# Optimization experiments

Hardware: AMD Instinct MI355X
Metric: run time of the kernel (lower is better)

Reference implementation:

```python
import jax, jax.numpy as jnp
import numpy as np

N = 50000
E = 1600000
IN_C = 256
HID = 32
HEADS = 4
NUM_CLASSES = 16
NEG_SLOPE = 0.2  # PyG GATConv default leaky_relu slope


def setup_inputs() -> dict:
    key = jax.random.key(0)
    ks = jax.random.split(key, 12)
    glorot = lambda k, shape: jax.random.normal(k, shape, jnp.float32) * jnp.sqrt(2.0 / (shape[0] + shape[-1]))
    x = jax.random.normal(ks[0], (N, IN_C), jnp.float32)
    edge_index = jax.random.randint(ks[1], (2, E), 0, N, jnp.int64)
    # layer 1: in -> hidden x heads, concat
    W1 = glorot(ks[2], (IN_C, HEADS * HID))
    att_src1 = glorot(ks[3], (HEADS, HID))
    att_dst1 = glorot(ks[4], (HEADS, HID))
    b1 = jnp.zeros((HEADS * HID,), jnp.float32)
    # layer 2: hidden*heads -> num_classes, 1 head, no concat
    W2 = glorot(ks[5], (HEADS * HID, NUM_CLASSES))
    att_src2 = glorot(ks[6], (1, NUM_CLASSES))
    att_dst2 = glorot(ks[7], (1, NUM_CLASSES))
    b2 = jnp.zeros((NUM_CLASSES,), jnp.float32)
    return {"x": x, "edge_index": edge_index, "W1": W1, "att_src1": att_src1,
            "att_dst1": att_dst1, "b1": b1, "W2": W2, "att_src2": att_src2,
            "att_dst2": att_dst2, "b2": b2}


def gat_conv(x, src, dst, W, a_src, a_dst, b, concat):
    # x: [N, F_in]; src/dst: [E'] (self-loops included); a_src/a_dst: [H, C]
    H, C = a_src.shape
    h = (x @ W).reshape(-1, H, C)                       # [N, H, C]
    alpha_s = jnp.sum(h * a_src[None], axis=-1)          # [N, H]
    alpha_d = jnp.sum(h * a_dst[None], axis=-1)          # [N, H]
    e = jax.nn.leaky_relu(alpha_s[src] + alpha_d[dst], NEG_SLOPE)  # [E', H]
    # segment softmax over edges grouped by destination node
    m = jax.ops.segment_max(e, dst, num_segments=N)      # [N, H]
    m = jnp.where(jnp.isfinite(m), m, 0.0)
    p = jnp.exp(e - m[dst])
    denom = jax.ops.segment_sum(p, dst, num_segments=N)  # [N, H]
    coef = p / (denom[dst] + 1e-16)                      # [E', H]
    msg = h[src] * coef[:, :, None]                      # [E', H, C]
    out = jax.ops.segment_sum(msg, dst, num_segments=N)  # [N, H, C]
    out = out.reshape(N, H * C) if concat else out.mean(axis=1)
    return out + b


def reference(x, edge_index, W1, att_src1, att_dst1, b1, W2, att_src2, att_dst2, b2):
    # PyG GATConv adds self-loops by default
    loops = jnp.arange(N, dtype=edge_index.dtype)
    src = jnp.concatenate([edge_index[0], loops])
    dst = jnp.concatenate([edge_index[1], loops])
    h = gat_conv(x, src, dst, W1, att_src1, att_dst1, b1, concat=True)
    h = jax.nn.elu(h)
    # dropout is identity in eval mode
    out = gat_conv(h, src, dst, W2, att_src2, att_dst2, b2, concat=False)
    return jax.nn.log_softmax(out, axis=1)
```

## Files before the change

### kernel.cpp

```cpp
#include <hip/hip_runtime.h>
#include <math.h>

#define INC   256
#define HIDALL 128
#define HEADS 4
#define HID   32
#define NCLS  16
#define NEG   0.2f
#define BSH   9
#define MAXBUCK 128
#define BCAP  24576

typedef __attribute__((ext_vector_type(8))) short short8_t;
typedef __attribute__((ext_vector_type(4))) float f32x4_t;

__device__ __forceinline__ float lrelu(float v) { return fmaxf(v, NEG * v); }

__device__ __forceinline__ float bflo(unsigned int v) { return __uint_as_float(v << 16); }
__device__ __forceinline__ float bfhi(unsigned int v) { return __uint_as_float(v & 0xFFFF0000u); }
__device__ __forceinline__ float bfhix(unsigned int v) { return __uint_as_float(v); }
__device__ __forceinline__ unsigned int f2bf(float f) {
  unsigned int v = __float_as_uint(f);
  return (v + 0x7FFFu + ((v >> 16) & 1u)) >> 16;
}
__device__ __forceinline__ unsigned int pack2(float a, float b) {
  return f2bf(a) | (f2bf(b) << 16);
}

__global__ void wt_k(const float* __restrict__ W, unsigned short* __restrict__ wtb) {
  int i = blockIdx.x * 256 + threadIdx.x;
  int k = i >> 7, c = i & 127;
  wtb[(((k >> 5) * 4 + ((k >> 3) & 3)) * 128 + c) * 8 + (k & 7)] =
      (unsigned short)f2bf(W[i]);
}

#define GM 64
__global__ __launch_bounds__(256) void gemm1_k(const float* __restrict__ x,
                                               const unsigned short* __restrict__ wtb,
                                               const float* __restrict__ asrc,
                                               const float* __restrict__ adst,
                                               unsigned short* __restrict__ h1,
                                               float* __restrict__ as1,
                                               float* __restrict__ ad1, int Nrows) {
  __shared__ unsigned short xs2[4][GM][8];
  __shared__ unsigned short wsm2[4][128][8];
  __shared__ unsigned short hs[GM][128];
  __shared__ float attL[2 * HIDALL];
  int t = threadIdx.x;
  int m0 = blockIdx.x * GM;
  int w = t >> 6, lane = t & 63;
  if (t < HIDALL) attL[t] = asrc[t];
  else attL[t] = adst[t - HIDALL];

  f32x4_t acc[8];
#pragma unroll
  for (int ct = 0; ct < 8; ++ct) acc[ct] = (f32x4_t){0.f, 0.f, 0.f, 0.f};

  int rowA = w * 16 + (lane & 15);
  int kg = lane >> 4;
  int cl = lane & 15;

  for (int ks = 0; ks < 8; ++ks) {
    int kc = ks * 32;
#pragma unroll
    for (int jj = 0; jj < 2; ++jj) {
      int u = t + jj * 256;
      int row = u >> 3, c4i = u & 7;
      int gr = m0 + row;
      float4 v = (gr < Nrows) ? *(const float4*)&x[(size_t)gr * INC + kc + c4i * 4]
                              : make_float4(0.f, 0.f, 0.f, 0.f);
      uint2 p;
      p.x = pack2(v.x, v.y);
      p.y = pack2(v.z, v.w);
      *(uint2*)&xs2[c4i >> 1][row][(c4i & 1) * 4] = p;
    }
    const unsigned short* wt = wtb + ks * 4096;
#pragma unroll
    for (int jj = 0; jj < 2; ++jj) {
      int u = t + jj * 256;
      *(uint4*)&((unsigned short*)wsm2)[u * 8] = *(const uint4*)&wt[u * 8];
    }
    __syncthreads();
    short8_t a = *(const short8_t*)&xs2[kg][rowA][0];
#pragma unroll
    for (int ct = 0; ct < 8; ++ct) {
      short8_t b = *(const short8_t*)&wsm2[kg][ct * 16 + cl][0];
      acc[ct] = __builtin_amdgcn_mfma_f32_16x16x32_bf16(a, b, acc[ct], 0, 0, 0);
    }
    __syncthreads();
  }
#pragma unroll
  for (int ct = 0; ct < 8; ++ct)
#pragma unroll
    for (int r = 0; r < 4; ++r)
      hs[w * 16 + (lane >> 4) * 4 + r][ct * 16 + cl] = (unsigned short)f2bf(acc[ct][r]);
  __syncthreads();
#pragma unroll
  for (int jj = 0; jj < 4; ++jj) {
    int u = t + jj * 256;
    int row = u >> 4, seg = u & 15;
    int gr = m0 + row;
    if (gr < Nrows)
      *(uint4*)&h1[(size_t)gr * HIDALL + seg * 8] = *(const uint4*)&hs[row][seg * 8];
  }
  {
    int row = t >> 2, h = t & 3;
    int gr = m0 + row;
    if (gr < Nrows) {
      float s = 0.f, dd = 0.f;
#pragma unroll
      for (int qq = 0; qq < 4; ++qq) {
        uint4 qv = *(const uint4*)&hs[row][h * 32 + qq * 8];
        int ab = h * 32 + qq * 8;
        s = fmaf(bflo(qv.x), attL[ab + 0], s);
        dd = fmaf(bflo(qv.x), attL[HIDALL + ab + 0], dd);
        s = fmaf(bfhi(qv.x), attL[ab + 1], s);
        dd = fmaf(bfhi(qv.x), attL[HIDALL + ab + 1], dd);
        s = fmaf(bflo(qv.y), attL[ab + 2], s);
        dd = fmaf(bflo(qv.y), attL[HIDALL + ab + 2], dd);
        s = fmaf(bfhi(qv.y), attL[ab + 3], s);
        dd = fmaf(bfhi(qv.y), attL[HIDALL + ab + 3], dd);
        s = fmaf(bflo(qv.z), attL[ab + 4], s);
        dd = fmaf(bflo(qv.z), attL[HIDALL + ab + 4], dd);
        s = fmaf(bfhi(qv.z), attL[ab + 5], s);
        dd = fmaf(bfhi(qv.z), attL[HIDALL + ab + 5], dd);
        s = fmaf(bflo(qv.w), attL[ab + 6], s);
        dd = fmaf(bflo(qv.w), attL[HIDALL + ab + 6], dd);
        s = fmaf(bfhi(qv.w), attL[ab + 7], s);
        dd = fmaf(bfhi(qv.w), attL[HIDALL + ab + 7], dd);
      }
      as1[(size_t)gr * 4 + h] = s;
      ad1[(size_t)gr * 4 + h] = dd;
    }
  }
}

#define S1_CH 8
__global__ __launch_bounds__(256) void stage1_k(const int* __restrict__ ei, int E,
                                                int* __restrict__ cursor,
                                                unsigned int* __restrict__ staging) {
  __shared__ int bh[MAXBUCK];
  __shared__ int bb[MAXBUCK];
  int t = threadIdx.x;
  if (t < MAXBUCK) bh[t] = 0;
  __syncthreads();
  int base = blockIdx.x * (256 * S1_CH);
  int s[S1_CH], d[S1_CH], r[S1_CH];
#pragma unroll
  for (int j = 0; j < S1_CH; ++j) {
    int e = base + t + j * 256;
    if (e < E) {
      s[j] = ei[e];
      d[j] = ei[(size_t)E + e];
      r[j] = atomicAdd(&bh[d[j] >> BSH], 1);
    } else {
      d[j] = -1;
    }
  }
  __syncthreads();
  if (t < MAXBUCK && bh[t]) bb[t] = atomicAdd(&cursor[t], bh[t]);
  __syncthreads();
#pragma unroll
  for (int j = 0; j < S1_CH; ++j) {
    if (d[j] >= 0) {
      int b = d[j] >> BSH;
      staging[(size_t)b * BCAP + bb[b] + r[j]] = ((unsigned)d[j] << 16) | (unsigned)s[j];
    }
  }
}

__global__ __launch_bounds__(MAXBUCK) void bscan_k(const int* __restrict__ cursor,
                                                   int* __restrict__ bucketOff) {
  __shared__ int v[MAXBUCK];
  int t = threadIdx.x;
  v[t] = cursor[t];
  __syncthreads();
  for (int off = 1; off < MAXBUCK; off <<= 1) {
    int x = (t >= off) ? v[t - off] : 0;
    __syncthreads();
    v[t] += x;
    __syncthreads();
  }
  bucketOff[t] = t ? v[t - 1] : 0;
  if (t == MAXBUCK - 1) bucketOff[MAXBUCK] = v[t];
}

__global__ __launch_bounds__(1024) void stage2_k(const unsigned int* __restrict__ staging,
                                                 const int* __restrict__ bucketOff,
                                                 int* __restrict__ rowptr,
                                                 int* __restrict__ esrc, int n, int lastb) {
  __shared__ int cnt[1 << BSH];
  __shared__ int cur[1 << BSH];
  int b = blockIdx.x, nb0 = b << BSH, t = threadIdx.x;
  if (t < (1 << BSH)) cnt[t] = 0;
  __syncthreads();
  int gbeg = bucketOff[b];
  int fill = bucketOff[b + 1] - gbeg;
  const unsigned int* st = staging + (size_t)b * BCAP;
  for (int i = t; i < fill; i += 1024)
    atomicAdd(&cnt[(st[i] >> 16) - nb0], 1);
  __syncthreads();
  for (int o = 1; o < (1 << BSH); o <<= 1) {
    int v = 0;
    if (t < (1 << BSH) && t >= o) v = cnt[t - o];
    __syncthreads();
    if (t < (1 << BSH)) cnt[t] += v;
    __syncthreads();
  }
  if (t < (1 << BSH)) {
    int excl = t ? cnt[t - 1] : 0;
    int node = nb0 + t;
    if (node < n) rowptr[node] = gbeg + excl;
    cur[t] = gbeg + excl;
  }
  if (b == lastb && t == 0) rowptr[n] = bucketOff[b + 1];
  __syncthreads();
  for (int i = t; i < fill; i += 1024) {
    unsigned v = st[i];
    int pos = atomicAdd(&cur[(v >> 16) - nb0], 1);
    esrc[pos] = (int)(v & 0xFFFFu);
  }
}

#define A1FMA(w_, u_)                                                      \
  a[0] = fmaf(w_, bflo(u_.x), a[0]); a[1] = fmaf(w_, bfhix(u_.x), a[1]);   \
  a[2] = fmaf(w_, bflo(u_.y), a[2]); a[3] = fmaf(w_, bfhix(u_.y), a[3]);   \
  a[4] = fmaf(w_, bflo(u_.z), a[4]); a[5] = fmaf(w_, bfhix(u_.z), a[5]);   \
  a[6] = fmaf(w_, bflo(u_.w), a[6]); a[7] = fmaf(w_, bfhix(u_.w), a[7]);

__global__ __launch_bounds__(256) void agg1_k(const int* __restrict__ rowptr,
                                              const int* __restrict__ esrc,
                                              const unsigned short* __restrict__ h1,
                                              const float* __restrict__ as1,
                                              const float* __restrict__ ad1,
                                              const float* __restrict__ b1,
                                              unsigned short* __restrict__ hin2b, int n) {
  int wid = (blockIdx.x * 256 + threadIdx.x) >> 6;
  int lane = threadIdx.x & 63;
  if (wid >= 2 * n) return;
  int d = wid >> 1, half = wid & 1;
  int beg = rowptr[d], end = rowptr[d + 1];
  int fb8 = lane & 7, q = lane >> 3;
  int fOff = half * 64 + fb8 * 8;
  int h = half * 2 + (fb8 >> 2);
  float adv_h = ad1[4 * (size_t)d + h];
  float ws = __expf(lrelu(as1[4 * (size_t)d + h] + adv_h));
  float den = 0.f;
  float a[8] = {0.f, 0.f, 0.f, 0.f, 0.f, 0.f, 0.f, 0.f};
  for (int i = beg + q; i < end; i += 32) {
    int e2 = i + 8, e3 = i + 16, e4 = i + 24;
    bool v2 = e2 < end, v3 = e3 < end, v4 = e4 < end;
    int s1 = esrc[i];
    int s2 = v2 ? esrc[e2] : s1;
    int s3 = v3 ? esrc[e3] : s1;
    int s4 = v4 ? esrc[e4] : s1;
    float av1 = as1[4 * (size_t)s1 + h];
    float av2 = as1[4 * (size_t)s2 + h];
    float av3 = as1[4 * (size_t)s3 + h];
    float av4 = as1[4 * (size_t)s4 + h];
    uint4 u1 = *(const uint4*)&h1[(size_t)s1 * HIDALL + fOff];
    uint4 u2 = *(const uint4*)&h1[(size_t)s2 * HIDALL + fOff];
    uint4 u3 = *(const uint4*)&h1[(size_t)s3 * HIDALL + fOff];
    uint4 u4 = *(const uint4*)&h1[(size_t)s4 * HIDALL + fOff];
    float w1 = __expf(lrelu(av1 + adv_h));
    float w2 = v2 ? __expf(lrelu(av2 + adv_h)) : 0.f;
    float w3 = v3 ? __expf(lrelu(av3 + adv_h)) : 0.f;
    float w4 = v4 ? __expf(lrelu(av4 + adv_h)) : 0.f;
    den += (w1 + w2) + (w3 + w4);
    A1FMA(w1, u1)
    A1FMA(w2, u2)
    A1FMA(w3, u3)
    A1FMA(w4, u4)
  }
#pragma unroll
  for (int off = 8; off <= 32; off <<= 1) den += __shfl_xor(den, off);
#pragma unroll
  for (int j = 0; j < 8; j++) {
    a[j] += __shfl_xor(a[j], 8);
    a[j] += __shfl_xor(a[j], 16);
    a[j] += __shfl_xor(a[j], 32);
  }
  if (q == 0) {
    uint4 ud = *(const uint4*)&h1[(size_t)d * HIDALL + fOff];
    den += ws;
    float inv = 1.f / (den + 1e-16f);
    const float* bp = &b1[fOff];
    float4 bb0 = *(const float4*)bp;
    float4 bb1 = *(const float4*)(bp + 4);
    float v[8];
    v[0] = fmaf(ws, bflo(ud.x), a[0]) * inv + bb0.x;
    v[1] = fmaf(ws, bfhi(ud.x), a[1]) * inv + bb0.y;
    v[2] = fmaf(ws, bflo(ud.y), a[2]) * inv + bb0.z;
    v[3] = fmaf(ws, bfhi(ud.y), a[3]) * inv + bb0.w;
    v[4] = fmaf(ws, bflo(ud.z), a[4]) * inv + bb1.x;
    v[5] = fmaf(ws, bfhi(ud.z), a[5]) * inv + bb1.y;
    v[6] = fmaf(ws, bflo(ud.w), a[6]) * inv + bb1.z;
    v[7] = fmaf(ws, bfhi(ud.w), a[7]) * inv + bb1.w;
#pragma unroll
    for (int j = 0; j < 8; j++) v[j] = v[j] > 0.f ? v[j] : (__expf(v[j]) - 1.f);
    uint4 pv;
    pv.x = pack2(v[0], v[1]);
    pv.y = pack2(v[2], v[3]);
    pv.z = pack2(v[4], v[5]);
    pv.w = pack2(v[6], v[7]);
    *(uint4*)&hin2b[(size_t)d * HIDALL + fOff] = pv;
  }
}

__global__ __launch_bounds__(256) void gemm2_k(const unsigned short* __restrict__ hin2b,
                                               const float* __restrict__ W2,
                                               const float* __restrict__ a2s,
                                               const float* __restrict__ a2d,
                                               unsigned int* __restrict__ h2x,
                                               float* __restrict__ ad2, int n) {
  __shared__ float wsm[128 * 16];
  __shared__ float hs[16][129];
  int t = threadIdx.x;
#pragma unroll
  for (int j = 0; j < 8; j++) wsm[t + j * 256] = W2[t + j * 256];
  int n0 = blockIdx.x * 16;
  const unsigned int* hw = (const unsigned int*)hin2b;
#pragma unroll
  for (int j = 0; j < 4; j++) {
    int u = t + j * 256;
    int r = u >> 6, cu = u & 63;
    int gn = n0 + r;
    unsigned v = (gn < n) ? hw[(size_t)gn * 64 + cu] : 0u;
    hs[r][cu * 2] = bflo(v);
    hs[r][cu * 2 + 1] = bfhi(v);
  }
  __syncthreads();
  int nl = t >> 4, c = t & 15;
  int gn = n0 + nl;
  float acc = 0.f;
#pragma unroll
  for (int k = 0; k < 128; k++) acc = fmaf(hs[nl][k], wsm[k * 16 + c], acc);
  float ps = acc * a2s[c];
  float pd = acc * a2d[c];
#pragma unroll
  for (int off = 8; off; off >>= 1) {
    ps += __shfl_xor(ps, off);
    pd += __shfl_xor(pd, off);
  }
  float other = __shfl_xor(acc, 1);
  if (gn < n) {
    if ((c & 1) == 0) h2x[(size_t)gn * 16 + (c >> 1)] = pack2(acc, other);
    if (c == 0) {
      h2x[(size_t)gn * 16 + 8] = __float_as_uint(ps);
      ad2[gn] = pd;
    }
  }
}

__global__ __launch_bounds__(256) void agg2_k(const int* __restrict__ rowptr,
                                              const int* __restrict__ esrc,
                                              const unsigned int* __restrict__ h2x,
                                              const float* __restrict__ ad2,
                                              const float* __restrict__ b2,
                                              float* __restrict__ out, int n) {
  int wid = (blockIdx.x * 256 + threadIdx.x) >> 6;
  int lane = threadIdx.x & 63;
  if (wid >= n) return;
  int d = wid;
  int beg = rowptr[d], end = rowptr[d + 1];
  int c2 = lane & 7, q = lane >> 3;
  float advd = ad2[d];
  float asd = __uint_as_float(h2x[(size_t)d * 16 + 8]);
  float ws = __expf(lrelu(asd + advd));
  float den = 0.f, a0 = 0.f, a1 = 0.f;
  for (int i = beg + q; i < end; i += 16) {
    int sA = esrc[i];
    const unsigned int* rA = &h2x[(size_t)sA * 16];
    float avA = __uint_as_float(rA[8]);
    unsigned uA = rA[c2];
    int i2 = i + 8;
    bool hasB = i2 < end;
    int sB = hasB ? esrc[i2] : sA;
    const unsigned int* rB = &h2x[(size_t)sB * 16];
    float avB = __uint_as_float(rB[8]);
    unsigned uB = rB[c2];
    float wA = __expf(lrelu(avA + advd));
    float wB = hasB ? __expf(lrelu(avB + advd)) : 0.f;
    den += wA + wB;
    a0 = fmaf(wA, bflo(uA), a0); a1 = fmaf(wA, bfhix(uA), a1);
    a0 = fmaf(wB, bflo(uB), a0); a1 = fmaf(wB, bfhix(uB), a1);
  }
#pragma unroll
  for (int off = 8; off <= 32; off <<= 1) {
    den += __shfl_xor(den, off);
    a0 += __shfl_xor(a0, off);
    a1 += __shfl_xor(a1, off);
  }
  unsigned ud = h2x[(size_t)d * 16 + c2];
  den += ws;
  a0 = fmaf(ws, bflo(ud), a0);
  a1 = fmaf(ws, bfhi(ud), a1);
  float inv = 1.f / (den + 1e-16f);
  float l0 = a0 * inv + b2[2 * c2];
  float l1 = a1 * inv + b2[2 * c2 + 1];
  float m = fmaxf(l0, l1);
#pragma unroll
  for (int off = 1; off <= 4; off <<= 1) m = fmaxf(m, __shfl_xor(m, off));
  float se = __expf(l0 - m) + __expf(l1 - m);
#pragma unroll
  for (int off = 1; off <= 4; off <<= 1) se += __shfl_xor(se, off);
  float lg = logf(se);
  if (q == 0) {
    float2 r = make_float2(l0 - m - lg, l1 - m - lg);
    *(float2*)&out[(size_t)d * NCLS + 2 * c2] = r;
  }
}

extern "C" void kernel_launch(void* const* d_in, const int* in_sizes, int n_in,
                              void* d_out, int out_size, void* d_ws, size_t ws_size,
                              hipStream_t stream) {
  const float* x = (const float*)d_in[0];
  const int* ei = (const int*)d_in[1];
  const float* W1 = (const float*)d_in[2];
  const float* asrc1 = (const float*)d_in[3];
  const float* adst1 = (const float*)d_in[4];
  const float* b1 = (const float*)d_in[5];
  const float* W2 = (const float*)d_in[6];
  const float* asrc2 = (const float*)d_in[7];
  const float* adst2 = (const float*)d_in[8];
  const float* b2 = (const float*)d_in[9];
  int N = in_sizes[0] / INC;
  int E = in_sizes[1] / 2;
  float* out = (float*)d_out;
  int nbuck = (N + (1 << BSH) - 1) >> BSH;

  char* ws = (char*)d_ws;
  size_t off = 0;
  auto alloc = [&](size_t bytes) {
    void* p = ws + off;
    off = (off + bytes + 255) & ~(size_t)255;
    return p;
  };
  unsigned short* h1 = (unsigned short*)alloc((size_t)N * HIDALL * 2);
  unsigned short* hin2b = (unsigned short*)alloc((size_t)N * HIDALL * 2);
  float* as1 = (float*)alloc((size_t)N * HEADS * 4);
  float* ad1 = (float*)alloc((size_t)N * HEADS * 4);
  unsigned int* h2x = (unsigned int*)alloc((size_t)N * 16 * 4);
  float* ad2 = (float*)alloc((size_t)N * 4);
  int* rowptr = (int*)alloc(((size_t)N + 1) * 4);
  int* cursor = (int*)alloc(MAXBUCK * 4);
  int* bucketOff = (int*)alloc((MAXBUCK + 1) * 4);
  int* esrc = (int*)alloc((size_t)E * 4);
  unsigned int* staging = (unsigned int*)alloc((size_t)MAXBUCK * BCAP * 4);
  unsigned short* wtb = (unsigned short*)alloc((size_t)INC * HIDALL * 2);

  hipMemsetAsync(cursor, 0, MAXBUCK * 4, stream);
  wt_k<<<(INC * HIDALL) / 256, 256, 0, stream>>>(W1, wtb);
  gemm1_k<<<(N + GM - 1) / GM, 256, 0, stream>>>(x, wtb, asrc1, adst1, h1, as1, ad1, N);
  stage1_k<<<(E + 256 * S1_CH - 1) / (256 * S1_CH), 256, 0, stream>>>(ei, E, cursor, staging);
  bscan_k<<<1, MAXBUCK, 0, stream>>>(cursor, bucketOff);
  stage2_k<<<nbuck, 1024, 0, stream>>>(staging, bucketOff, rowptr, esrc, N, nbuck - 1);
  agg1_k<<<(2 * N + 3) / 4, 256, 0, stream>>>(rowptr, esrc, h1, as1, ad1, b1, hin2b, N);
  gemm2_k<<<(N + 15) / 16, 256, 0, stream>>>(hin2b, W2, asrc2, adst2, h2x, ad2, N);
  agg2_k<<<(N + 3) / 4, 256, 0, stream>>>(rowptr, esrc, h2x, ad2, b2, out, N);
}
```

Baseline: 183.0 us.

## Pad CSR rows to multiples of 32 with sentinel node and drop bucket scan

Each destination row's edge list is padded to a multiple of 32 entries. The padding points to an extra sentinel node whose attention logit is -1e30, so its softmax weight is zero. The aggregation loops can then drop their per-edge bounds checks, and the per-bucket fixed-capacity layout removes the separate bucket-scan kernel. agg1 also switches to packed two-wide FMA accumulation. The costs are extra wasted gathers on padding entries (an average of about 16 per row against roughly 33 real edges), a larger esrc buffer, and a hard cap (PCAP) on padded edges per bucket.

```diff
diff --git a/kernel.cpp b/kernel.cpp
--- a/kernel.cpp
+++ b/kernel.cpp
@@ -10,9 +10,11 @@
 #define BSH   9
 #define MAXBUCK 128
 #define BCAP  24576
+#define PCAP  40960
 
 typedef __attribute__((ext_vector_type(8))) short short8_t;
 typedef __attribute__((ext_vector_type(4))) float f32x4_t;
+typedef __attribute__((ext_vector_type(2))) float f32x2;
 
 __device__ __forceinline__ float lrelu(float v) { return fmaxf(v, NEG * v); }
 
@@ -27,8 +29,12 @@
   return f2bf(a) | (f2bf(b) << 16);
 }
 
-__global__ void wt_k(const float* __restrict__ W, unsigned short* __restrict__ wtb) {
+__global__ void wt_k(const float* __restrict__ W, unsigned short* __restrict__ wtb,
+                     float* __restrict__ as1, unsigned int* __restrict__ h2x, int n) {
   int i = blockIdx.x * 256 + threadIdx.x;
+  if (i < 4) as1[4 * (size_t)n + i] = -1e30f;
+  if (i >= 4 && i < 12) h2x[16 * (size_t)n + (i - 4)] = 0u;
+  if (i == 12) h2x[16 * (size_t)n + 8] = __float_as_uint(-1e30f);
   int k = i >> 7, c = i & 127;
   wtb[(((k >> 5) * 4 + ((k >> 3) & 3)) * 128 + c) * 8 + (k & 7)] =
       (unsigned short)f2bf(W[i]);
@@ -169,66 +175,61 @@
   }
 }
 
-__global__ __launch_bounds__(MAXBUCK) void bscan_k(const int* __restrict__ cursor,
-                                                   int* __restrict__ bucketOff) {
-  __shared__ int v[MAXBUCK];
-  int t = threadIdx.x;
-  v[t] = cursor[t];
-  __syncthreads();
-  for (int off = 1; off < MAXBUCK; off <<= 1) {
-    int x = (t >= off) ? v[t - off] : 0;
-    __syncthreads();
-    v[t] += x;
-    __syncthreads();
-  }
-  bucketOff[t] = t ? v[t - 1] : 0;
-  if (t == MAXBUCK - 1) bucketOff[MAXBUCK] = v[t];
-}
-
 __global__ __launch_bounds__(1024) void stage2_k(const unsigned int* __restrict__ staging,
-                                                 const int* __restrict__ bucketOff,
+                                                 const int* __restrict__ cursor,
                                                  int* __restrict__ rowptr,
-                                                 int* __restrict__ esrc, int n, int lastb) {
+                                                 int* __restrict__ rowend,
+                                                 int* __restrict__ esrc, int n) {
   __shared__ int cnt[1 << BSH];
-  __shared__ int cur[1 << BSH];
+  __shared__ int pfx[1 << BSH];
+  __shared__ int curw[1 << BSH];
   int b = blockIdx.x, nb0 = b << BSH, t = threadIdx.x;
   if (t < (1 << BSH)) cnt[t] = 0;
   __syncthreads();
-  int gbeg = bucketOff[b];
-  int fill = bucketOff[b + 1] - gbeg;
+  int fill = cursor[b];
   const unsigned int* st = staging + (size_t)b * BCAP;
   for (int i = t; i < fill; i += 1024)
     atomicAdd(&cnt[(st[i] >> 16) - nb0], 1);
   __syncthreads();
+  if (t < (1 << BSH)) pfx[t] = (cnt[t] + 31) & ~31;
+  __syncthreads();
   for (int o = 1; o < (1 << BSH); o <<= 1) {
     int v = 0;
-    if (t < (1 << BSH) && t >= o) v = cnt[t - o];
+    if (t < (1 << BSH) && t >= o) v = pfx[t - o];
     __syncthreads();
-    if (t < (1 << BSH)) cnt[t] += v;
+    if (t < (1 << BSH)) pfx[t] += v;
     __syncthreads();
   }
   if (t < (1 << BSH)) {
-    int excl = t ? cnt[t - 1] : 0;
+    int padDeg = (cnt[t] + 31) & ~31;
+    int rp = b * PCAP + pfx[t] - padDeg;
     int node = nb0 + t;
-    if (node < n) rowptr[node] = gbeg + excl;
-    cur[t] = gbeg + excl;
-  }
-  if (b == lastb && t == 0) rowptr[n] = bucketOff[b + 1];
+    if (node < n) {
+      rowptr[node] = rp;
+      rowend[node] = rp + padDeg;
+    }
+    curw[t] = rp;
+    for (int i = cnt[t]; i < padDeg; ++i) esrc[rp + i] = n;
+  }
   __syncthreads();
   for (int i = t; i < fill; i += 1024) {
     unsigned v = st[i];
-    int pos = atomicAdd(&cur[(v >> 16) - nb0], 1);
+    int pos = atomicAdd(&curw[(v >> 16) - nb0], 1);
     esrc[pos] = (int)(v & 0xFFFFu);
   }
 }
 
-#define A1FMA(w_, u_)                                                      \
-  a[0] = fmaf(w_, bflo(u_.x), a[0]); a[1] = fmaf(w_, bfhix(u_.x), a[1]);   \
-  a[2] = fmaf(w_, bflo(u_.y), a[2]); a[3] = fmaf(w_, bfhix(u_.y), a[3]);   \
-  a[4] = fmaf(w_, bflo(u_.z), a[4]); a[5] = fmaf(w_, bfhix(u_.z), a[5]);   \
-  a[6] = fmaf(w_, bflo(u_.w), a[6]); a[7] = fmaf(w_, bfhix(u_.w), a[7]);
+#define A1PK(w_, u_)                                                            \
+  {                                                                             \
+    f32x2 wv = {w_, w_};                                                        \
+    a2[0] = __builtin_elementwise_fma(wv, (f32x2){bflo(u_.x), bfhix(u_.x)}, a2[0]); \
+    a2[1] = __builtin_elementwise_fma(wv, (f32x2){bflo(u_.y), bfhix(u_.y)}, a2[1]); \
+    a2[2] = __builtin_elementwise_fma(wv, (f32x2){bflo(u_.z), bfhix(u_.z)}, a2[2]); \
+    a2[3] = __builtin_elementwise_fma(wv, (f32x2){bflo(u_.w), bfhix(u_.w)}, a2[3]); \
+  }
 
 __global__ __launch_bounds__(256) void agg1_k(const int* __restrict__ rowptr,
+                                              const int* __restrict__ rowend,
                                               const int* __restrict__ esrc,
                                               const unsigned short* __restrict__ h1,
                                               const float* __restrict__ as1,
@@ -239,21 +240,20 @@
   int lane = threadIdx.x & 63;
   if (wid >= 2 * n) return;
   int d = wid >> 1, half = wid & 1;
-  int beg = rowptr[d], end = rowptr[d + 1];
+  int beg = rowptr[d], end = rowend[d];
   int fb8 = lane & 7, q = lane >> 3;
   int fOff = half * 64 + fb8 * 8;
   int h = half * 2 + (fb8 >> 2);
   float adv_h = ad1[4 * (size_t)d + h];
   float ws = __expf(lrelu(as1[4 * (size_t)d + h] + adv_h));
   float den = 0.f;
-  float a[8] = {0.f, 0.f, 0.f, 0.f, 0.f, 0.f, 0.f, 0.f};
+  f32x2 a2[4];
+  a2[0] = a2[1] = a2[2] = a2[3] = (f32x2){0.f, 0.f};
   for (int i = beg + q; i < end; i += 32) {
-    int e2 = i + 8, e3 = i + 16, e4 = i + 24;
-    bool v2 = e2 < end, v3 = e3 < end, v4 = e4 < end;
     int s1 = esrc[i];
-    int s2 = v2 ? esrc[e2] : s1;
-    int s3 = v3 ? esrc[e3] : s1;
-    int s4 = v4 ? esrc[e4] : s1;
+    int s2 = esrc[i + 8];
+    int s3 = esrc[i + 16];
+    int s4 = esrc[i + 24];
     float av1 = as1[4 * (size_t)s1 + h];
     float av2 = as1[4 * (size_t)s2 + h];
     float av3 = as1[4 * (size_t)s3 + h];
@@ -263,15 +263,17 @@
     uint4 u3 = *(const uint4*)&h1[(size_t)s3 * HIDALL + fOff];
     uint4 u4 = *(const uint4*)&h1[(size_t)s4 * HIDALL + fOff];
     float w1 = __expf(lrelu(av1 + adv_h));
-    float w2 = v2 ? __expf(lrelu(av2 + adv_h)) : 0.f;
-    float w3 = v3 ? __expf(lrelu(av3 + adv_h)) : 0.f;
-    float w4 = v4 ? __expf(lrelu(av4 + adv_h)) : 0.f;
+    float w2 = __expf(lrelu(av2 + adv_h));
+    float w3 = __expf(lrelu(av3 + adv_h));
+    float w4 = __expf(lrelu(av4 + adv_h));
     den += (w1 + w2) + (w3 + w4);
-    A1FMA(w1, u1)
-    A1FMA(w2, u2)
-    A1FMA(w3, u3)
-    A1FMA(w4, u4)
-  }
+    A1PK(w1, u1)
+    A1PK(w2, u2)
+    A1PK(w3, u3)
+    A1PK(w4, u4)
+  }
+  float a[8] = {a2[0].x, a2[0].y, a2[1].x, a2[1].y,
+                a2[2].x, a2[2].y, a2[3].x, a2[3].y};
 #pragma unroll
   for (int off = 8; off <= 32; off <<= 1) den += __shfl_xor(den, off);
 #pragma unroll
@@ -353,6 +355,7 @@
 }
 
 __global__ __launch_bounds__(256) void agg2_k(const int* __restrict__ rowptr,
+                                              const int* __restrict__ rowend,
                                               const int* __restrict__ esrc,
                                               const unsigned int* __restrict__ h2x,
                                               const float* __restrict__ ad2,
@@ -362,7 +365,7 @@
   int lane = threadIdx.x & 63;
   if (wid >= n) return;
   int d = wid;
-  int beg = rowptr[d], end = rowptr[d + 1];
+  int beg = rowptr[d], end = rowend[d];
   int c2 = lane & 7, q = lane >> 3;
   float advd = ad2[d];
   float asd = __uint_as_float(h2x[(size_t)d * 16 + 8]);
@@ -373,14 +376,12 @@
     const unsigned int* rA = &h2x[(size_t)sA * 16];
     float avA = __uint_as_float(rA[8]);
     unsigned uA = rA[c2];
-    int i2 = i + 8;
-    bool hasB = i2 < end;
-    int sB = hasB ? esrc[i2] : sA;
+    int sB = esrc[i + 8];
     const unsigned int* rB = &h2x[(size_t)sB * 16];
     float avB = __uint_as_float(rB[8]);
     unsigned uB = rB[c2];
     float wA = __expf(lrelu(avA + advd));
-    float wB = hasB ? __expf(lrelu(avB + advd)) : 0.f;
+    float wB = __expf(lrelu(avB + advd));
     den += wA + wB;
     a0 = fmaf(wA, bflo(uA), a0); a1 = fmaf(wA, bfhix(uA), a1);
     a0 = fmaf(wB, bflo(uB), a0); a1 = fmaf(wB, bfhix(uB), a1);
@@ -436,26 +437,25 @@
     off = (off + bytes + 255) & ~(size_t)255;
     return p;
   };
-  unsigned short* h1 = (unsigned short*)alloc((size_t)N * HIDALL * 2);
+  unsigned short* h1 = (unsigned short*)alloc((size_t)(N + 1) * HIDALL * 2);
   unsigned short* hin2b = (unsigned short*)alloc((size_t)N * HIDALL * 2);
-  float* as1 = (float*)alloc((size_t)N * HEADS * 4);
+  float* as1 = (float*)alloc((size_t)(N + 1) * HEADS * 4);
   float* ad1 = (float*)alloc((size_t)N * HEADS * 4);
-  unsigned int* h2x = (unsigned int*)alloc((size_t)N * 16 * 4);
+  unsigned int* h2x = (unsigned int*)alloc((size_t)(N + 1) * 16 * 4);
   float* ad2 = (float*)alloc((size_t)N * 4);
-  int* rowptr = (int*)alloc(((size_t)N + 1) * 4);
+  int* rowptr = (int*)alloc((size_t)N * 4);
+  int* rowend = (int*)alloc((size_t)N * 4);
   int* cursor = (int*)alloc(MAXBUCK * 4);
-  int* bucketOff = (int*)alloc((MAXBUCK + 1) * 4);
-  int* esrc = (int*)alloc((size_t)E * 4);
+  int* esrc = (int*)alloc((size_t)MAXBUCK * PCAP * 4);
   unsigned int* staging = (unsigned int*)alloc((size_t)MAXBUCK * BCAP * 4);
   unsigned short* wtb = (unsigned short*)alloc((size_t)INC * HIDALL * 2);
 
   hipMemsetAsync(cursor, 0, MAXBUCK * 4, stream);
-  wt_k<<<(INC * HIDALL) / 256, 256, 0, stream>>>(W1, wtb);
+  wt_k<<<(INC * HIDALL) / 256, 256, 0, stream>>>(W1, wtb, as1, h2x, N);
   gemm1_k<<<(N + GM - 1) / GM, 256, 0, stream>>>(x, wtb, asrc1, adst1, h1, as1, ad1, N);
   stage1_k<<<(E + 256 * S1_CH - 1) / (256 * S1_CH), 256, 0, stream>>>(ei, E, cursor, staging);
-  bscan_k<<<1, MAXBUCK, 0, stream>>>(cursor, bucketOff);
-  stage2_k<<<nbuck, 1024, 0, stream>>>(staging, bucketOff, rowptr, esrc, N, nbuck - 1);
-  agg1_k<<<(2 * N + 3) / 4, 256, 0, stream>>>(rowptr, esrc, h1, as1, ad1, b1, hin2b, N);
+  stage2_k<<<nbuck, 1024, 0, stream>>>(staging, cursor, rowptr, rowend, esrc, N);
+  agg1_k<<<(2 * N + 3) / 4, 256, 0, stream>>>(rowptr, rowend, esrc, h1, as1, ad1, b1, hin2b, N);
   gemm2_k<<<(N + 15) / 16, 256, 0, stream>>>(hin2b, W2, asrc2, adst2, h2x, ad2, N);
-  agg2_k<<<(N + 3) / 4, 256, 0, stream>>>(rowptr, esrc, h2x, ad2, b2, out, N);
-}
+  agg2_k<<<(N + 3) / 4, 256, 0, stream>>>(rowptr, rowend, esrc, h2x, ad2, b2, out, N);
+}
```

Measured after the change: 176.2 us. 1.04x faster.
